# Kernel optimization log

Hardware: AMD Instinct MI355X
Metric: run time of the kernel (lower is better)

The kernel has to match this reference:

```python
import jax, jax.numpy as jnp
import numpy as np

H, L, N = 512, 2048, 64  # channels, seq len, SSM state size


def _make_dplr_hippo(n):
    # make_HiPPO / make_NPLR_HiPPO / make_DPLR_HiPPO from the source
    p0 = np.sqrt(1.0 + 2.0 * np.arange(n))
    A = p0[:, None] * p0[None, :]
    A = np.tril(A) - np.diag(np.arange(n))
    nhippo = -A
    P = np.sqrt(np.arange(n) + 0.5)
    B = np.sqrt(2.0 * np.arange(n) + 1.0)
    S = nhippo + P[:, None] * P[None, :]
    S_diag = np.diagonal(S)
    Lam_re = np.mean(S_diag) * np.ones_like(S_diag)
    Lam_im, V = jnp.linalg.eigh(jnp.asarray(S, jnp.complex64) * (-1j))
    Pc = V.conj().T @ jnp.asarray(P, jnp.complex64)
    Bc = V.conj().T @ jnp.asarray(B, jnp.complex64)
    return (jnp.asarray(Lam_re, jnp.float32), jnp.asarray(Lam_im, jnp.float32),
            Pc, Bc)


def setup_inputs() -> dict:
    key = jax.random.key(0)
    k_u, k_c, k_s = jax.random.split(key, 3)
    Lre, Lim, Pc, Bc = _make_dplr_hippo(N)
    tile = lambda v: jnp.tile(v[None, :], (H, 1)).astype(jnp.float32)  # (H,N)
    return {
        "u": jax.random.normal(k_u, (L, H), dtype=jnp.float32),
        "x0_re": jnp.zeros((N, H), jnp.float32),
        "x0_im": jnp.zeros((N, H), jnp.float32),
        "Lambda_re": tile(Lre),
        "Lambda_im": tile(Lim),
        "P_re": tile(Pc.real), "P_im": tile(Pc.imag),
        "B_re": tile(Bc.real), "B_im": tile(Bc.imag),
        "C": jax.random.normal(k_c, (H, N, 2), jnp.float32) * (0.5 ** 0.5),
        "D": jnp.ones((H, 1), jnp.float32),
        "log_step": jax.random.uniform(k_s, (H, 1), jnp.float32,
                                       minval=np.log(1e-3), maxval=np.log(1e-1)),
    }


def _discretize(Lam, P, B, Ct, step):
    # discrete_DPLR with Q = P (as in setup); per-channel, vmapped over H.
    n = Lam.shape[0]
    I = jnp.eye(n, dtype=jnp.complex64)
    A = jnp.diag(Lam) - P[:, None] * P.conj()[None, :]
    A0 = (2.0 / step) * I + A
    Dd = jnp.diag(1.0 / (2.0 / step - Lam))
    Qc = P.conj()[None, :]            # (1,N)
    P2 = P[:, None]                   # (N,1)
    A1 = Dd - (Dd @ P2) * (1.0 / (1.0 + Qc @ Dd @ P2)) * (Qc @ Dd)
    Ab = A1 @ A0                      # (N,N)
    Bb = 2.0 * (A1 @ B[:, None])[:, 0]
    AbL = jnp.linalg.matrix_power(Ab, L)
    Cb = (Ct[None, :] @ jnp.linalg.inv(I - AbL).conj()).conj()[0]
    return Ab, Bb, Cb


def _forward(u, x0_re, x0_im, Lambda_re, Lambda_im, P_re, P_im,
             B_re, B_im, C, D, log_step):
    Lam = jnp.clip(Lambda_re, None, -0.0001) + 1j * Lambda_im  # (H,N)
    Pc = P_re + 1j * P_im
    Bc = B_re + 1j * B_im
    Cc = C[..., 0] + 1j * C[..., 1]
    step = jnp.exp(log_step)[:, 0]                              # (H,)
    Ab, Bb, Cb = jax.vmap(_discretize)(Lam, Pc, Bc, Cc, step)   # (H,N,N),(H,N),(H,N)

    x0 = jnp.transpose(x0_re + 1j * x0_im)                      # (H,N) complex

    def body(x, u_t):  # x: (H,N) complex, u_t: (H,)
        x = jnp.einsum('hnm,hm->hn', Ab, x) + Bb * u_t[:, None]
        y = jnp.einsum('hn,hn->h', Cb, x)
        return x, y.real

    _, ys = jax.lax.scan(body, x0, u)                           # ys: (L,H)
    return ys + u * D[:, 0][None, :]                            # (L,H) float32


def reference(u, x0_re, x0_im, Lambda_re, Lambda_im, P_re, P_im,
              B_re, B_im, C, D, log_step):
    return _forward(u, x0_re, x0_im, Lambda_re, Lambda_im, P_re, P_im,
                    B_re, B_im, C, D, log_step)
```

## Files before the change

kernel.cpp:

```cpp
#include <hip/hip_runtime.h>

#define HH 512
#define LL 2048
#define NN 64
#define TT 64
#define CC 32
#define NLDA 68
#define SP 72

typedef __attribute__((ext_vector_type(8))) short bf16x8_t;
typedef __attribute__((ext_vector_type(4))) float floatx4;

__device__ __forceinline__ float2 cmul(float2 a, float2 b) {
    return make_float2(a.x * b.x - a.y * b.y, a.x * b.y + a.y * b.x);
}
__device__ __forceinline__ float2 crecip(float2 a) {
    float id = 1.0f / (a.x * a.x + a.y * a.y);
    return make_float2(a.x * id, -a.y * id);
}
template <int CTRL>
__device__ __forceinline__ float dpp_mov(float x) {
    return __int_as_float(__builtin_amdgcn_update_dpp(
        0, __float_as_int(x), CTRL, 0xf, 0xf, true));
}
__device__ __forceinline__ float wave_sum_bcast(float x) {
    x += dpp_mov<0x111>(x);
    x += dpp_mov<0x112>(x);
    x += dpp_mov<0x114>(x);
    x += dpp_mov<0x118>(x);
    x += dpp_mov<0x142>(x);
    x += dpp_mov<0x143>(x);
    return __int_as_float(__builtin_amdgcn_readlane(__float_as_int(x), 63));
}
__device__ __forceinline__ float rlane(float x, int i) {
    return __int_as_float(__builtin_amdgcn_readlane(__float_as_int(x), i));
}
__device__ __forceinline__ unsigned short f2bf(float f) {
    unsigned int u = __float_as_uint(f);
    u += 0x7FFFu + ((u >> 16) & 1u);
    return (unsigned short)(u >> 16);
}
__device__ __forceinline__ float bf2f(unsigned short s) {
    return __uint_as_float(((unsigned int)s) << 16);
}

__device__ __forceinline__ void closed_form(
    int h, int n,
    const float* __restrict__ Lre, const float* __restrict__ Lim,
    const float* __restrict__ Pre, const float* __restrict__ Pim,
    const float* __restrict__ Bre, const float* __restrict__ Bim,
    const float* __restrict__ logstep,
    float2& da, float2& DPv, float2& tv, float2& bb) {
    float step = expf(logstep[h]);
    float as = 2.0f / step;
    float lr = fminf(Lre[h * NN + n], -1e-4f);
    float li = Lim[h * NN + n];
    float2 a = make_float2(as + lr, li);
    float2 Dn = crecip(make_float2(as - lr, -li));
    float2 P = make_float2(Pre[h * NN + n], Pim[h * NN + n]);
    float2 Bv = make_float2(Bre[h * NN + n], Bim[h * NN + n]);
    float2 cP = make_float2(P.x, -P.y);
    float p2 = P.x * P.x + P.y * P.y;
    float2 rt = cmul(cmul(cP, Dn), Bv);
    float2 e = make_float2(wave_sum_bcast(Dn.x * p2), wave_sum_bcast(Dn.y * p2));
    float2 rv = make_float2(wave_sum_bcast(rt.x), wave_sum_bcast(rt.y));
    float2 cc = crecip(make_float2(1.0f + e.x, e.y));
    da = cmul(Dn, a);
    DPv = cmul(Dn, P);
    float2 tmp = cmul(cc, make_float2(da.x - e.x, da.y - e.y));
    tv = cmul(cP, make_float2(1.0f + tmp.x, tmp.y));
    float2 crv = cmul(cc, rv);
    float2 cd = cmul(crv, DPv);
    float2 db = cmul(Dn, Bv);
    bb = make_float2(2.0f * (db.x - cd.x), 2.0f * (db.y - cd.y));
}

__device__ __forceinline__ void pack_tiles(
    unsigned short* mRh, unsigned short* mRl,
    unsigned short* mIh, unsigned short* mIl,
    unsigned short* mTRh, unsigned short* mTRl,
    unsigned short* mTIh, unsigned short* mTIl,
    int w, int lm, int q, const float Cr[4][4], const float Ci[4][4]) {
    #pragma unroll
    for (int nt = 0; nt < 4; ++nt) {
        const int c = nt * 16 + lm;
        unsigned short hr[4], lr_[4], hi_[4], li_[4];
        #pragma unroll
        for (int reg = 0; reg < 4; ++reg) {
            const float xr = Cr[nt][reg], xi = Ci[nt][reg];
            hr[reg] = f2bf(xr); lr_[reg] = f2bf(xr - bf2f(hr[reg]));
            hi_[reg] = f2bf(xi); li_[reg] = f2bf(xi - bf2f(hi_[reg]));
            const int r = 16 * w + 4 * q + reg;
            mRh[r * SP + c] = hr[reg]; mRl[r * SP + c] = lr_[reg];
            mIh[r * SP + c] = hi_[reg]; mIl[r * SP + c] = li_[reg];
        }
        const int tb = c * SP + 16 * w + 4 * q;
        *(ushort4*)&mTRh[tb] = make_ushort4(hr[0], hr[1], hr[2], hr[3]);
        *(ushort4*)&mTRl[tb] = make_ushort4(lr_[0], lr_[1], lr_[2], lr_[3]);
        *(ushort4*)&mTIh[tb] = make_ushort4(hi_[0], hi_[1], hi_[2], hi_[3]);
        *(ushort4*)&mTIl[tb] = make_ushort4(li_[0], li_[1], li_[2], li_[3]);
    }
}

extern "C" __global__ void __launch_bounds__(256, 2)
k_fusedA(const float* __restrict__ Lre, const float* __restrict__ Lim,
         const float* __restrict__ Pre, const float* __restrict__ Pim,
         const float* __restrict__ Bre, const float* __restrict__ Bim,
         const float* __restrict__ Cmat, const float* __restrict__ logstep,
         const float* __restrict__ u,
         float2* __restrict__ wM, float2* __restrict__ wCb,
         float2* __restrict__ wP) {
    extern __shared__ __align__(16) char smem[];
    const int tid = threadIdx.x;

    if (blockIdx.x < HH) {
        const int h = blockIdx.x;
        unsigned short* mRh  = (unsigned short*)smem;
        unsigned short* mRl  = mRh + 64 * SP;
        unsigned short* mIh  = mRl + 64 * SP;
        unsigned short* mIl  = mIh + 64 * SP;
        unsigned short* mTRh = mIl + 64 * SP;
        unsigned short* mTRl = mTRh + 64 * SP;
        unsigned short* mTIh = mTRl + 64 * SP;
        unsigned short* mTIl = mTIh + 64 * SP;
        float* Nr = (float*)smem;
        float* Ni = Nr + 64 * NLDA;
        float2* sda  = (float2*)(smem + 73728);
        float2* sDP  = sda + NN;
        float2* st   = sDP + NN;
        float2* sBb  = st + NN;
        float2* srhs = sBb + NN;
        float2* sx   = srhs + NN;
        float2* pp   = sx + NN;

        const int w = tid >> 6;
        const int lane = tid & 63;
        const int lm = lane & 15, q = lane >> 4;

        if (tid < NN) {
            float2 da, DPv, tv, bb;
            closed_form(h, tid, Lre, Lim, Pre, Pim, Bre, Bim, logstep,
                        da, DPv, tv, bb);
            sda[tid] = da; sDP[tid] = DPv; st[tid] = tv; sBb[tid] = bb;
            srhs[tid] = make_float2(Cmat[h * NN * 2 + tid * 2],
                                    -Cmat[h * NN * 2 + tid * 2 + 1]);
        }
        __syncthreads();

        {
            float Cr[4][4], Ci[4][4];
            #pragma unroll
            for (int nt = 0; nt < 4; ++nt) {
                const int c = nt * 16 + lm;
                const float2 tc = st[c];
                #pragma unroll
                for (int reg = 0; reg < 4; ++reg) {
                    const int r = 16 * w + 4 * q + reg;
                    const float2 dp = sDP[r];
                    float vr = -(dp.x * tc.x - dp.y * tc.y);
                    float vi = -(dp.x * tc.y + dp.y * tc.x);
                    if (r == c) { vr += sda[r].x; vi += sda[r].y; }
                    Cr[nt][reg] = vr; Ci[nt][reg] = vi;
                }
            }
            pack_tiles(mRh, mRl, mIh, mIl, mTRh, mTRl, mTIh, mTIl,
                       w, lm, q, Cr, Ci);
        }
        __syncthreads();

        const int arow = (16 * w + lm) * SP + q * 8;
        for (int it = 0; it < 11; ++it) {
            floatx4 z4 = {0.f, 0.f, 0.f, 0.f};
            floatx4 aP[4] = {z4, z4, z4, z4};
            floatx4 aQ[4] = {z4, z4, z4, z4};
            floatx4 aC[4] = {z4, z4, z4, z4};
            for (int k2 = 0; k2 < 2; ++k2) {
                const int ao = arow + k2 * 32;
                const bf16x8_t ARh = *(const bf16x8_t*)&mRh[ao];
                const bf16x8_t ARl = *(const bf16x8_t*)&mRl[ao];
                const bf16x8_t AIh = *(const bf16x8_t*)&mIh[ao];
                const bf16x8_t AIl = *(const bf16x8_t*)&mIl[ao];
                bf16x8_t BRh[4], BRl[4], BIh[4], BIl[4];
                #pragma unroll
                for (int nt = 0; nt < 4; ++nt) {
                    const int bo = (nt * 16 + lm) * SP + k2 * 32 + q * 8;
                    BRh[nt] = *(const bf16x8_t*)&mTRh[bo];
                    BRl[nt] = *(const bf16x8_t*)&mTRl[bo];
                    BIh[nt] = *(const bf16x8_t*)&mTIh[bo];
                    BIl[nt] = *(const bf16x8_t*)&mTIl[bo];
                }
                #pragma unroll
                for (int nt = 0; nt < 4; ++nt) {
                    aP[nt] = __builtin_amdgcn_mfma_f32_16x16x32_bf16(ARh, BRh[nt], aP[nt], 0, 0, 0);
                    aP[nt] = __builtin_amdgcn_mfma_f32_16x16x32_bf16(ARh, BRl[nt], aP[nt], 0, 0, 0);
                    aP[nt] = __builtin_amdgcn_mfma_f32_16x16x32_bf16(ARl, BRh[nt], aP[nt], 0, 0, 0);
                    aQ[nt] = __builtin_amdgcn_mfma_f32_16x16x32_bf16(AIh, BIh[nt], aQ[nt], 0, 0, 0);
                    aQ[nt] = __builtin_amdgcn_mfma_f32_16x16x32_bf16(AIh, BIl[nt], aQ[nt], 0, 0, 0);
                    aQ[nt] = __builtin_amdgcn_mfma_f32_16x16x32_bf16(AIl, BIh[nt], aQ[nt], 0, 0, 0);
                    aC[nt] = __builtin_amdgcn_mfma_f32_16x16x32_bf16(ARh, BIh[nt], aC[nt], 0, 0, 0);
                    aC[nt] = __builtin_amdgcn_mfma_f32_16x16x32_bf16(ARh, BIl[nt], aC[nt], 0, 0, 0);
                    aC[nt] = __builtin_amdgcn_mfma_f32_16x16x32_bf16(ARl, BIh[nt], aC[nt], 0, 0, 0);
                    aC[nt] = __builtin_amdgcn_mfma_f32_16x16x32_bf16(AIh, BRh[nt], aC[nt], 0, 0, 0);
                    aC[nt] = __builtin_amdgcn_mfma_f32_16x16x32_bf16(AIh, BRl[nt], aC[nt], 0, 0, 0);
                    aC[nt] = __builtin_amdgcn_mfma_f32_16x16x32_bf16(AIl, BRh[nt], aC[nt], 0, 0, 0);
                }
            }
            __syncthreads();
            if (it < 10) {
                float Cr[4][4], Ci[4][4];
                #pragma unroll
                for (int nt = 0; nt < 4; ++nt)
                    #pragma unroll
                    for (int reg = 0; reg < 4; ++reg) {
                        Cr[nt][reg] = aP[nt][reg] - aQ[nt][reg];
                        Ci[nt][reg] = aC[nt][reg];
                    }
                pack_tiles(mRh, mRl, mIh, mIl, mTRh, mTRl, mTIh, mTIl,
                           w, lm, q, Cr, Ci);
                __syncthreads();
                if (it == 5) {
                    for (int idx = tid; idx < NN * NN; idx += 256) {
                        const int c = idx >> 6, k = idx & 63;
                        wM[h * NN * NN + idx] = make_float2(
                            bf2f(mTRh[c * SP + k]) + bf2f(mTRl[c * SP + k]),
                            bf2f(mTIh[c * SP + k]) + bf2f(mTIl[c * SP + k]));
                    }
                }
            } else {
                #pragma unroll
                for (int nt = 0; nt < 4; ++nt) {
                    const int c = nt * 16 + lm;
                    #pragma unroll
                    for (int reg = 0; reg < 4; ++reg) {
                        const int r = 16 * w + 4 * q + reg;
                        Nr[r * NLDA + c] = aP[nt][reg] - aQ[nt][reg];
                        Ni[r * NLDA + c] = aC[nt][reg];
                    }
                }
                __syncthreads();
            }
        }

        if (tid < NN) sx[tid] = srhs[tid];
        __syncthreads();
        for (int itn = 0; itn < 24; ++itn) {
            const int i = tid & 63, qq = tid >> 6;
            float pr = 0.0f, pi = 0.0f;
            #pragma unroll 4
            for (int jj = 0; jj < 16; ++jj) {
                const int j = qq * 16 + jj;
                const float nr = Nr[j * NLDA + i], ni = Ni[j * NLDA + i];
                const float2 xj = sx[j];
                pr += nr * xj.x - ni * xj.y;
                pi += nr * xj.y + ni * xj.x;
            }
            pp[qq * 64 + i] = make_float2(pr, pi);
            __syncthreads();
            if (tid < NN) {
                const float2 a0 = pp[tid], a1 = pp[64 + tid];
                const float2 a2 = pp[128 + tid], a3 = pp[192 + tid];
                sx[tid] = make_float2(
                    srhs[tid].x + a0.x + a1.x + a2.x + a3.x,
                    srhs[tid].y + a0.y + a1.y + a2.y + a3.y);
            }
            __syncthreads();
        }
        if (tid < NN) wCb[h * NN + tid] = sx[tid];
    } else {
        const int h = blockIdx.x - HH;
        float2* sG  = (float2*)smem;
        float*  su  = (float*)(smem + 32768);
        float2* sda = (float2*)(smem + 40960);
        float2* sDP = sda + NN;
        float2* st  = sDP + NN;
        float2* sBb = st + NN;

        const int wv = tid >> 6, lane = tid & 63;
        for (int idx = tid; idx < LL; idx += 256)
            su[idx] = u[idx * HH + h];
        if (tid < NN) {
            float2 da, DPv, tv, bb;
            closed_form(h, tid, Lre, Lim, Pre, Pim, Bre, Bim, logstep,
                        da, DPv, tv, bb);
            sda[tid] = da; sDP[tid] = DPv; st[tid] = tv; sBb[tid] = bb;
        }
        __syncthreads();

        if (tid < 64) {
            const float2 da = sda[lane], DP = sDP[lane], tt = st[lane];
            float Gr = sBb[lane].x, Gi = sBb[lane].y;
            for (int m = 0; m < TT; ++m) {
                sG[m * NN + lane] = make_float2(Gr, Gi);
                float c1 = tt.x * Gr - tt.y * Gi;
                float c2 = tt.x * Gi + tt.y * Gr;
                c1 += dpp_mov<0x111>(c1); c2 += dpp_mov<0x111>(c2);
                c1 += dpp_mov<0x112>(c1); c2 += dpp_mov<0x112>(c2);
                c1 += dpp_mov<0x114>(c1); c2 += dpp_mov<0x114>(c2);
                c1 += dpp_mov<0x118>(c1); c2 += dpp_mov<0x118>(c2);
                c1 += dpp_mov<0x142>(c1); c2 += dpp_mov<0x142>(c2);
                c1 += dpp_mov<0x143>(c1); c2 += dpp_mov<0x143>(c2);
                const float S1 = rlane(c1, 63);
                const float S2 = rlane(c2, 63);
                float nGr = da.x * Gr - da.y * Gi - (DP.x * S1 - DP.y * S2);
                float nGi = da.x * Gi + da.y * Gr - (DP.x * S2 + DP.y * S1);
                Gr = nGr; Gi = nGi;
            }
        }
        __syncthreads();

        float accr[8] = {}, acci[8] = {};
        for (int j = 0; j < TT; ++j) {
            const float2 g = sG[(TT - 1 - j) * NN + lane];
            #pragma unroll
            for (int qc = 0; qc < 8; ++qc) {
                const float uv = su[((wv * 8 + qc) << 6) + j];
                accr[qc] += g.x * uv; acci[qc] += g.y * uv;
            }
        }
        #pragma unroll
        for (int qc = 0; qc < 8; ++qc)
            wP[(h * CC + wv * 8 + qc) * NN + lane] = make_float2(accr[qc], acci[qc]);
    }
}

extern "C" __global__ void __launch_bounds__(256, 2)
k_fusedB(const float* __restrict__ Lre, const float* __restrict__ Lim,
         const float* __restrict__ Pre, const float* __restrict__ Pim,
         const float* __restrict__ Bre, const float* __restrict__ Bim,
         const float* __restrict__ logstep,
         const float* __restrict__ u, const float* __restrict__ Dvec,
         const float* __restrict__ x0_re, const float* __restrict__ x0_im,
         const float2* __restrict__ wM, const float2* __restrict__ wCb,
         const float2* __restrict__ wP, float* __restrict__ out) {
    extern __shared__ __align__(16) char smem[];
    unsigned short* sVr  = (unsigned short*)smem;
    unsigned short* sVi  = (unsigned short*)(smem + 9216);
    unsigned short* sXrh = (unsigned short*)(smem + 18432);
    unsigned short* sXrl = (unsigned short*)(smem + 23040);
    unsigned short* sXih = (unsigned short*)(smem + 27648);
    unsigned short* sXil = (unsigned short*)(smem + 32256);
    float*          su   = (float*)(smem + 36864);
    float*          sK   = (float*)(smem + 45056);
    float*          y0   = (float*)(smem + 45312);

    const int h = blockIdx.x;
    const int tid = threadIdx.x;
    const int wv = tid >> 6, lane = tid & 63;
    const int lm = lane & 15, q = lane >> 4;

    if (wv == 0) {
        float2 da, DP, tt, Bb;
        closed_form(h, lane, Lre, Lim, Pre, Pim, Bre, Bim, logstep,
                    da, DP, tt, Bb);
        const float2 Cb = wCb[h * NN + lane];
        float Gr = Bb.x, Gi = Bb.y;
        float vr = Cb.x, vi = Cb.y;
        for (int m = 0; m < TT; ++m) {
            float ch[5];
            ch[0] = Cb.x * Gr - Cb.y * Gi;
            ch[1] = tt.x * Gr - tt.y * Gi;
            ch[2] = tt.x * Gi + tt.y * Gr;
            ch[3] = vr * DP.x - vi * DP.y;
            ch[4] = vr * DP.y + vi * DP.x;
            #pragma unroll
            for (int c = 0; c < 5; ++c) ch[c] += dpp_mov<0x111>(ch[c]);
            #pragma unroll
            for (int c = 0; c < 5; ++c) ch[c] += dpp_mov<0x112>(ch[c]);
            #pragma unroll
            for (int c = 0; c < 5; ++c) ch[c] += dpp_mov<0x114>(ch[c]);
            #pragma unroll
            for (int c = 0; c < 5; ++c) ch[c] += dpp_mov<0x118>(ch[c]);
            #pragma unroll
            for (int c = 0; c < 5; ++c) ch[c] += dpp_mov<0x142>(ch[c]);
            #pragma unroll
            for (int c = 0; c < 5; ++c) ch[c] += dpp_mov<0x143>(ch[c]);
            const float S0 = rlane(ch[0], 63);
            const float S1 = rlane(ch[1], 63);
            const float S2 = rlane(ch[2], 63);
            const float S3 = rlane(ch[3], 63);
            const float S4 = rlane(ch[4], 63);
            if (lane == 0) sK[m] = S0;
            float nGr = da.x * Gr - da.y * Gi - (DP.x * S1 - DP.y * S2);
            float nGi = da.x * Gi + da.y * Gr - (DP.x * S2 + DP.y * S1);
            Gr = nGr; Gi = nGi;
            float nvr = da.x * vr - da.y * vi - (S3 * tt.x - S4 * tt.y);
            float nvi = da.x * vi + da.y * vr - (S3 * tt.y + S4 * tt.x);
            vr = nvr; vi = nvi;
            sVr[m * SP + lane] = f2bf(vr);
            sVi[m * SP + lane] = f2bf(-vi);
        }
    } else if (wv == 1) {
        float Mr[NN], Mi[NN];
        const float2* __restrict__ wMh = wM + h * NN * NN;
        #pragma unroll
        for (int j = 0; j < NN; ++j) {
            const float2 v = wMh[j * NN + lane];
            Mr[j] = v.x; Mi[j] = v.y;
        }
        float xr = x0_re[lane * HH + h], xi = x0_im[lane * HH + h];
        {
            const unsigned short hr = f2bf(xr), hi_ = f2bf(xi);
            sXrh[lane] = hr;  sXrl[lane] = f2bf(xr - bf2f(hr));
            sXih[lane] = hi_; sXil[lane] = f2bf(xi - bf2f(hi_));
        }
        float2 pe_next = wP[(h * CC + 0) * NN + lane];
        for (int c = 1; c < CC; ++c) {
            const float2 pe = pe_next;
            if (c < CC - 1) pe_next = wP[(h * CC + c) * NN + lane];
            float ar[4] = {0.f, 0.f, 0.f, 0.f};
            float ai[4] = {0.f, 0.f, 0.f, 0.f};
            #pragma unroll
            for (int j = 0; j < NN; ++j) {
                const float xjr = rlane(xr, j);
                const float xji = rlane(xi, j);
                ar[j & 3] = fmaf(Mr[j], xjr, ar[j & 3]);
                ar[j & 3] = fmaf(-Mi[j], xji, ar[j & 3]);
                ai[j & 3] = fmaf(Mr[j], xji, ai[j & 3]);
                ai[j & 3] = fmaf(Mi[j], xjr, ai[j & 3]);
            }
            xr = ((ar[0] + ar[1]) + (ar[2] + ar[3])) + pe.x;
            xi = ((ai[0] + ai[1]) + (ai[2] + ai[3])) + pe.y;
            const unsigned short hr = f2bf(xr), hi_ = f2bf(xi);
            sXrh[c * SP + lane] = hr;  sXrl[c * SP + lane] = f2bf(xr - bf2f(hr));
            sXih[c * SP + lane] = hi_; sXil[c * SP + lane] = f2bf(xi - bf2f(hi_));
        }
    } else {
        for (int idx = tid - 128; idx < LL; idx += 128)
            su[idx] = u[idx * HH + h];
    }
    __syncthreads();

    {
        const float Dh = Dvec[h];
        float acc[8] = {};
        for (int s = 0; s < TT; ++s) {
            const int d = lane - s;
            const float kv = (d >= 0) ? sK[d < 0 ? 0 : d] : 0.0f;
            #pragma unroll
            for (int qc = 0; qc < 8; ++qc)
                acc[qc] += kv * su[((wv * 8 + qc) << 6) + s];
        }
        #pragma unroll
        for (int qc = 0; qc < 8; ++qc) {
            const int c = wv * 8 + qc;
            y0[c * 65 + lane] = acc[qc] + Dh * su[c * 64 + lane];
        }
    }
    __syncthreads();

    floatx4 z4 = {0.f, 0.f, 0.f, 0.f};
    floatx4 acc2[2] = {z4, z4};
    #pragma unroll
    for (int k2 = 0; k2 < 2; ++k2) {
        const int ak = (16 * wv + lm) * SP + k2 * 32 + q * 8;
        const bf16x8_t aVr = *(const bf16x8_t*)&sVr[ak];
        const bf16x8_t aVi = *(const bf16x8_t*)&sVi[ak];
        #pragma unroll
        for (int nt = 0; nt < 2; ++nt) {
            const int bk = (nt * 16 + lm) * SP + k2 * 32 + q * 8;
            const bf16x8_t bRh = *(const bf16x8_t*)&sXrh[bk];
            const bf16x8_t bRl = *(const bf16x8_t*)&sXrl[bk];
            const bf16x8_t bIh = *(const bf16x8_t*)&sXih[bk];
            const bf16x8_t bIl = *(const bf16x8_t*)&sXil[bk];
            acc2[nt] = __builtin_amdgcn_mfma_f32_16x16x32_bf16(aVr, bRh, acc2[nt], 0, 0, 0);
            acc2[nt] = __builtin_amdgcn_mfma_f32_16x16x32_bf16(aVr, bRl, acc2[nt], 0, 0, 0);
            acc2[nt] = __builtin_amdgcn_mfma_f32_16x16x32_bf16(aVi, bIh, acc2[nt], 0, 0, 0);
            acc2[nt] = __builtin_amdgcn_mfma_f32_16x16x32_bf16(aVi, bIl, acc2[nt], 0, 0, 0);
        }
    }
    #pragma unroll
    for (int nt = 0; nt < 2; ++nt) {
        #pragma unroll
        for (int reg = 0; reg < 4; ++reg) {
            const int c = nt * 16 + lm;
            const int t = 16 * wv + 4 * q + reg;
            out[(c * TT + t) * HH + h] = acc2[nt][reg] + y0[c * 65 + t];
        }
    }
}

extern "C" void kernel_launch(void* const* d_in, const int* in_sizes, int n_in,
                              void* d_out, int out_size, void* d_ws, size_t ws_size,
                              hipStream_t stream) {
    const float* u    = (const float*)d_in[0];
    const float* x0re = (const float*)d_in[1];
    const float* x0im = (const float*)d_in[2];
    const float* Lre  = (const float*)d_in[3];
    const float* Lim  = (const float*)d_in[4];
    const float* Pre  = (const float*)d_in[5];
    const float* Pim  = (const float*)d_in[6];
    const float* Bre  = (const float*)d_in[7];
    const float* Bim  = (const float*)d_in[8];
    const float* C    = (const float*)d_in[9];
    const float* Dv   = (const float*)d_in[10];
    const float* lst  = (const float*)d_in[11];

    float2* wM  = (float2*)d_ws;
    float2* wP  = wM + HH * NN * NN;
    float2* wCb = wP + HH * CC * NN;
    float* out = (float*)d_out;

    hipLaunchKernelGGL(k_fusedA, dim3(2 * HH), dim3(256), 78848, stream,
                       Lre, Lim, Pre, Pim, Bre, Bim, C, lst, u,
                       wM, wCb, wP);
    hipLaunchKernelGGL(k_fusedB, dim3(HH), dim3(256), 53632, stream,
                       Lre, Lim, Pre, Pim, Bre, Bim, lst, u, Dv,
                       x0re, x0im, wM, wCb, wP, out);
}
```

Baseline: 227.1 us.

## Move chunk-input state computation into kernel B and cut Neumann iterations

```diff
diff --git a/kernel.cpp b/kernel.cpp
--- a/kernel.cpp
+++ b/kernel.cpp
@@ -107,220 +107,162 @@
          const float* __restrict__ Pre, const float* __restrict__ Pim,
          const float* __restrict__ Bre, const float* __restrict__ Bim,
          const float* __restrict__ Cmat, const float* __restrict__ logstep,
-         const float* __restrict__ u,
-         float2* __restrict__ wM, float2* __restrict__ wCb,
-         float2* __restrict__ wP) {
+         float2* __restrict__ wM, float2* __restrict__ wCb) {
     extern __shared__ __align__(16) char smem[];
     const int tid = threadIdx.x;
-
-    if (blockIdx.x < HH) {
-        const int h = blockIdx.x;
-        unsigned short* mRh  = (unsigned short*)smem;
-        unsigned short* mRl  = mRh + 64 * SP;
-        unsigned short* mIh  = mRl + 64 * SP;
-        unsigned short* mIl  = mIh + 64 * SP;
-        unsigned short* mTRh = mIl + 64 * SP;
-        unsigned short* mTRl = mTRh + 64 * SP;
-        unsigned short* mTIh = mTRl + 64 * SP;
-        unsigned short* mTIl = mTIh + 64 * SP;
-        float* Nr = (float*)smem;
-        float* Ni = Nr + 64 * NLDA;
-        float2* sda  = (float2*)(smem + 73728);
-        float2* sDP  = sda + NN;
-        float2* st   = sDP + NN;
-        float2* sBb  = st + NN;
-        float2* srhs = sBb + NN;
-        float2* sx   = srhs + NN;
-        float2* pp   = sx + NN;
-
-        const int w = tid >> 6;
-        const int lane = tid & 63;
-        const int lm = lane & 15, q = lane >> 4;
-
-        if (tid < NN) {
-            float2 da, DPv, tv, bb;
-            closed_form(h, tid, Lre, Lim, Pre, Pim, Bre, Bim, logstep,
-                        da, DPv, tv, bb);
-            sda[tid] = da; sDP[tid] = DPv; st[tid] = tv; sBb[tid] = bb;
-            srhs[tid] = make_float2(Cmat[h * NN * 2 + tid * 2],
-                                    -Cmat[h * NN * 2 + tid * 2 + 1]);
+    const int h = blockIdx.x;
+
+    unsigned short* mRh  = (unsigned short*)smem;
+    unsigned short* mRl  = mRh + 64 * SP;
+    unsigned short* mIh  = mRl + 64 * SP;
+    unsigned short* mIl  = mIh + 64 * SP;
+    unsigned short* mTRh = mIl + 64 * SP;
+    unsigned short* mTRl = mTRh + 64 * SP;
+    unsigned short* mTIh = mTRl + 64 * SP;
+    unsigned short* mTIl = mTIh + 64 * SP;
+    float* Nr = (float*)smem;
+    float* Ni = Nr + 64 * NLDA;
+    float2* sda  = (float2*)(smem + 73728);
+    float2* sDP  = sda + NN;
+    float2* st   = sDP + NN;
+    float2* sBb  = st + NN;
+    float2* srhs = sBb + NN;
+    float2* sx   = srhs + NN;
+    float2* pp   = sx + NN;
+
+    const int w = tid >> 6;
+    const int lane = tid & 63;
+    const int lm = lane & 15, q = lane >> 4;
+
+    if (tid < NN) {
+        float2 da, DPv, tv, bb;
+        closed_form(h, tid, Lre, Lim, Pre, Pim, Bre, Bim, logstep,
+                    da, DPv, tv, bb);
+        sda[tid] = da; sDP[tid] = DPv; st[tid] = tv; sBb[tid] = bb;
+        srhs[tid] = make_float2(Cmat[h * NN * 2 + tid * 2],
+                                -Cmat[h * NN * 2 + tid * 2 + 1]);
+    }
+    __syncthreads();
+
+    {
+        float Cr[4][4], Ci[4][4];
+        #pragma unroll
+        for (int nt = 0; nt < 4; ++nt) {
+            const int c = nt * 16 + lm;
+            const float2 tc = st[c];
+            #pragma unroll
+            for (int reg = 0; reg < 4; ++reg) {
+                const int r = 16 * w + 4 * q + reg;
+                const float2 dp = sDP[r];
+                float vr = -(dp.x * tc.x - dp.y * tc.y);
+                float vi = -(dp.x * tc.y + dp.y * tc.x);
+                if (r == c) { vr += sda[r].x; vi += sda[r].y; }
+                Cr[nt][reg] = vr; Ci[nt][reg] = vi;
+            }
+        }
+        pack_tiles(mRh, mRl, mIh, mIl, mTRh, mTRl, mTIh, mTIl,
+                   w, lm, q, Cr, Ci);
+    }
+    __syncthreads();
+
+    const int arow = (16 * w + lm) * SP + q * 8;
+    for (int it = 0; it < 11; ++it) {
+        floatx4 z4 = {0.f, 0.f, 0.f, 0.f};
+        floatx4 aP[4] = {z4, z4, z4, z4};
+        floatx4 aQ[4] = {z4, z4, z4, z4};
+        floatx4 aC[4] = {z4, z4, z4, z4};
+        for (int k2 = 0; k2 < 2; ++k2) {
+            const int ao = arow + k2 * 32;
+            const bf16x8_t ARh = *(const bf16x8_t*)&mRh[ao];
+            const bf16x8_t ARl = *(const bf16x8_t*)&mRl[ao];
+            const bf16x8_t AIh = *(const bf16x8_t*)&mIh[ao];
+            const bf16x8_t AIl = *(const bf16x8_t*)&mIl[ao];
+            bf16x8_t BRh[4], BRl[4], BIh[4], BIl[4];
+            #pragma unroll
+            for (int nt = 0; nt < 4; ++nt) {
+                const int bo = (nt * 16 + lm) * SP + k2 * 32 + q * 8;
+                BRh[nt] = *(const bf16x8_t*)&mTRh[bo];
+                BRl[nt] = *(const bf16x8_t*)&mTRl[bo];
+                BIh[nt] = *(const bf16x8_t*)&mTIh[bo];
+                BIl[nt] = *(const bf16x8_t*)&mTIl[bo];
+            }
+            #pragma unroll
+            for (int nt = 0; nt < 4; ++nt) {
+                aP[nt] = __builtin_amdgcn_mfma_f32_16x16x32_bf16(ARh, BRh[nt], aP[nt], 0, 0, 0);
+                aP[nt] = __builtin_amdgcn_mfma_f32_16x16x32_bf16(ARh, BRl[nt], aP[nt], 0, 0, 0);
+                aP[nt] = __builtin_amdgcn_mfma_f32_16x16x32_bf16(ARl, BRh[nt], aP[nt], 0, 0, 0);
+                aQ[nt] = __builtin_amdgcn_mfma_f32_16x16x32_bf16(AIh, BIh[nt], aQ[nt], 0, 0, 0);
+                aQ[nt] = __builtin_amdgcn_mfma_f32_16x16x32_bf16(AIh, BIl[nt], aQ[nt], 0, 0, 0);
+                aQ[nt] = __builtin_amdgcn_mfma_f32_16x16x32_bf16(AIl, BIh[nt], aQ[nt], 0, 0, 0);
+                aC[nt] = __builtin_amdgcn_mfma_f32_16x16x32_bf16(ARh, BIh[nt], aC[nt], 0, 0, 0);
+                aC[nt] = __builtin_amdgcn_mfma_f32_16x16x32_bf16(ARh, BIl[nt], aC[nt], 0, 0, 0);
+                aC[nt] = __builtin_amdgcn_mfma_f32_16x16x32_bf16(ARl, BIh[nt], aC[nt], 0, 0, 0);
+                aC[nt] = __builtin_amdgcn_mfma_f32_16x16x32_bf16(AIh, BRh[nt], aC[nt], 0, 0, 0);
+                aC[nt] = __builtin_amdgcn_mfma_f32_16x16x32_bf16(AIh, BRl[nt], aC[nt], 0, 0, 0);
+                aC[nt] = __builtin_amdgcn_mfma_f32_16x16x32_bf16(AIl, BRh[nt], aC[nt], 0, 0, 0);
+            }
         }
         __syncthreads();
-
-        {
+        if (it < 10) {
             float Cr[4][4], Ci[4][4];
+            #pragma unroll
+            for (int nt = 0; nt < 4; ++nt)
+                #pragma unroll
+                for (int reg = 0; reg < 4; ++reg) {
+                    Cr[nt][reg] = aP[nt][reg] - aQ[nt][reg];
+                    Ci[nt][reg] = aC[nt][reg];
+                }
+            pack_tiles(mRh, mRl, mIh, mIl, mTRh, mTRl, mTIh, mTIl,
+                       w, lm, q, Cr, Ci);
+            __syncthreads();
+            if (it == 5) {
+                for (int idx = tid; idx < NN * NN; idx += 256) {
+                    const int c = idx >> 6, k = idx & 63;
+                    wM[h * NN * NN + idx] = make_float2(
+                        bf2f(mTRh[c * SP + k]) + bf2f(mTRl[c * SP + k]),
+                        bf2f(mTIh[c * SP + k]) + bf2f(mTIl[c * SP + k]));
+                }
+            }
+        } else {
             #pragma unroll
             for (int nt = 0; nt < 4; ++nt) {
                 const int c = nt * 16 + lm;
-                const float2 tc = st[c];
                 #pragma unroll
                 for (int reg = 0; reg < 4; ++reg) {
                     const int r = 16 * w + 4 * q + reg;
-                    const float2 dp = sDP[r];
-                    float vr = -(dp.x * tc.x - dp.y * tc.y);
-                    float vi = -(dp.x * tc.y + dp.y * tc.x);
-                    if (r == c) { vr += sda[r].x; vi += sda[r].y; }
-                    Cr[nt][reg] = vr; Ci[nt][reg] = vi;
+                    Nr[r * NLDA + c] = aP[nt][reg] - aQ[nt][reg];
+                    Ni[r * NLDA + c] = aC[nt][reg];
                 }
             }
-            pack_tiles(mRh, mRl, mIh, mIl, mTRh, mTRl, mTIh, mTIl,
-                       w, lm, q, Cr, Ci);
-        }
+            __syncthreads();
+        }
+    }
+
+    if (tid < NN) sx[tid] = srhs[tid];
+    __syncthreads();
+    for (int itn = 0; itn < 16; ++itn) {
+        const int i = tid & 63, qq = tid >> 6;
+        float pr = 0.0f, pi = 0.0f;
+        #pragma unroll 4
+        for (int jj = 0; jj < 16; ++jj) {
+            const int j = qq * 16 + jj;
+            const float nr = Nr[j * NLDA + i], ni = Ni[j * NLDA + i];
+            const float2 xj = sx[j];
+            pr += nr * xj.x - ni * xj.y;
+            pi += nr * xj.y + ni * xj.x;
+        }
+        pp[qq * 64 + i] = make_float2(pr, pi);
         __syncthreads();
-
-        const int arow = (16 * w + lm) * SP + q * 8;
-        for (int it = 0; it < 11; ++it) {
-            floatx4 z4 = {0.f, 0.f, 0.f, 0.f};
-            floatx4 aP[4] = {z4, z4, z4, z4};
-            floatx4 aQ[4] = {z4, z4, z4, z4};
-            floatx4 aC[4] = {z4, z4, z4, z4};
-            for (int k2 = 0; k2 < 2; ++k2) {
-                const int ao = arow + k2 * 32;
-                const bf16x8_t ARh = *(const bf16x8_t*)&mRh[ao];
-                const bf16x8_t ARl = *(const bf16x8_t*)&mRl[ao];
-                const bf16x8_t AIh = *(const bf16x8_t*)&mIh[ao];
-                const bf16x8_t AIl = *(const bf16x8_t*)&mIl[ao];
-                bf16x8_t BRh[4], BRl[4], BIh[4], BIl[4];
-                #pragma unroll
-                for (int nt = 0; nt < 4; ++nt) {
-                    const int bo = (nt * 16 + lm) * SP + k2 * 32 + q * 8;
-                    BRh[nt] = *(const bf16x8_t*)&mTRh[bo];
-                    BRl[nt] = *(const bf16x8_t*)&mTRl[bo];
-                    BIh[nt] = *(const bf16x8_t*)&mTIh[bo];
-                    BIl[nt] = *(const bf16x8_t*)&mTIl[bo];
-                }
-                #pragma unroll
-                for (int nt = 0; nt < 4; ++nt) {
-                    aP[nt] = __builtin_amdgcn_mfma_f32_16x16x32_bf16(ARh, BRh[nt], aP[nt], 0, 0, 0);
-                    aP[nt] = __builtin_amdgcn_mfma_f32_16x16x32_bf16(ARh, BRl[nt], aP[nt], 0, 0, 0);
-                    aP[nt] = __builtin_amdgcn_mfma_f32_16x16x32_bf16(ARl, BRh[nt], aP[nt], 0, 0, 0);
-                    aQ[nt] = __builtin_amdgcn_mfma_f32_16x16x32_bf16(AIh, BIh[nt], aQ[nt], 0, 0, 0);
-                    aQ[nt] = __builtin_amdgcn_mfma_f32_16x16x32_bf16(AIh, BIl[nt], aQ[nt], 0, 0, 0);
-                    aQ[nt] = __builtin_amdgcn_mfma_f32_16x16x32_bf16(AIl, BIh[nt], aQ[nt], 0, 0, 0);
-                    aC[nt] = __builtin_amdgcn_mfma_f32_16x16x32_bf16(ARh, BIh[nt], aC[nt], 0, 0, 0);
-                    aC[nt] = __builtin_amdgcn_mfma_f32_16x16x32_bf16(ARh, BIl[nt], aC[nt], 0, 0, 0);
-                    aC[nt] = __builtin_amdgcn_mfma_f32_16x16x32_bf16(ARl, BIh[nt], aC[nt], 0, 0, 0);
-                    aC[nt] = __builtin_amdgcn_mfma_f32_16x16x32_bf16(AIh, BRh[nt], aC[nt], 0, 0, 0);
-                    aC[nt] = __builtin_amdgcn_mfma_f32_16x16x32_bf16(AIh, BRl[nt], aC[nt], 0, 0, 0);
-                    aC[nt] = __builtin_amdgcn_mfma_f32_16x16x32_bf16(AIl, BRh[nt], aC[nt], 0, 0, 0);
-                }
-            }
-            __syncthreads();
-            if (it < 10) {
-                float Cr[4][4], Ci[4][4];
-                #pragma unroll
-                for (int nt = 0; nt < 4; ++nt)
-                    #pragma unroll
-                    for (int reg = 0; reg < 4; ++reg) {
-                        Cr[nt][reg] = aP[nt][reg] - aQ[nt][reg];
-                        Ci[nt][reg] = aC[nt][reg];
-                    }
-                pack_tiles(mRh, mRl, mIh, mIl, mTRh, mTRl, mTIh, mTIl,
-                           w, lm, q, Cr, Ci);
-                __syncthreads();
-                if (it == 5) {
-                    for (int idx = tid; idx < NN * NN; idx += 256) {
-                        const int c = idx >> 6, k = idx & 63;
-                        wM[h * NN * NN + idx] = make_float2(
-                            bf2f(mTRh[c * SP + k]) + bf2f(mTRl[c * SP + k]),
-                            bf2f(mTIh[c * SP + k]) + bf2f(mTIl[c * SP + k]));
-                    }
-                }
-            } else {
-                #pragma unroll
-                for (int nt = 0; nt < 4; ++nt) {
-                    const int c = nt * 16 + lm;
-                    #pragma unroll
-                    for (int reg = 0; reg < 4; ++reg) {
-                        const int r = 16 * w + 4 * q + reg;
-                        Nr[r * NLDA + c] = aP[nt][reg] - aQ[nt][reg];
-                        Ni[r * NLDA + c] = aC[nt][reg];
-                    }
-                }
-                __syncthreads();
-            }
-        }
-
-        if (tid < NN) sx[tid] = srhs[tid];
+        if (tid < NN) {
+            const float2 a0 = pp[tid], a1 = pp[64 + tid];
+            const float2 a2 = pp[128 + tid], a3 = pp[192 + tid];
+            sx[tid] = make_float2(
+                srhs[tid].x + a0.x + a1.x + a2.x + a3.x,
+                srhs[tid].y + a0.y + a1.y + a2.y + a3.y);
+        }
         __syncthreads();
-        for (int itn = 0; itn < 24; ++itn) {
-            const int i = tid & 63, qq = tid >> 6;
-            float pr = 0.0f, pi = 0.0f;
-            #pragma unroll 4
-            for (int jj = 0; jj < 16; ++jj) {
-                const int j = qq * 16 + jj;
-                const float nr = Nr[j * NLDA + i], ni = Ni[j * NLDA + i];
-                const float2 xj = sx[j];
-                pr += nr * xj.x - ni * xj.y;
-                pi += nr * xj.y + ni * xj.x;
-            }
-            pp[qq * 64 + i] = make_float2(pr, pi);
-            __syncthreads();
-            if (tid < NN) {
-                const float2 a0 = pp[tid], a1 = pp[64 + tid];
-                const float2 a2 = pp[128 + tid], a3 = pp[192 + tid];
-                sx[tid] = make_float2(
-                    srhs[tid].x + a0.x + a1.x + a2.x + a3.x,
-                    srhs[tid].y + a0.y + a1.y + a2.y + a3.y);
-            }
-            __syncthreads();
-        }
-        if (tid < NN) wCb[h * NN + tid] = sx[tid];
-    } else {
-        const int h = blockIdx.x - HH;
-        float2* sG  = (float2*)smem;
-        float*  su  = (float*)(smem + 32768);
-        float2* sda = (float2*)(smem + 40960);
-        float2* sDP = sda + NN;
-        float2* st  = sDP + NN;
-        float2* sBb = st + NN;
-
-        const int wv = tid >> 6, lane = tid & 63;
-        for (int idx = tid; idx < LL; idx += 256)
-            su[idx] = u[idx * HH + h];
-        if (tid < NN) {
-            float2 da, DPv, tv, bb;
-            closed_form(h, tid, Lre, Lim, Pre, Pim, Bre, Bim, logstep,
-                        da, DPv, tv, bb);
-            sda[tid] = da; sDP[tid] = DPv; st[tid] = tv; sBb[tid] = bb;
-        }
-        __syncthreads();
-
-        if (tid < 64) {
-            const float2 da = sda[lane], DP = sDP[lane], tt = st[lane];
-            float Gr = sBb[lane].x, Gi = sBb[lane].y;
-            for (int m = 0; m < TT; ++m) {
-                sG[m * NN + lane] = make_float2(Gr, Gi);
-                float c1 = tt.x * Gr - tt.y * Gi;
-                float c2 = tt.x * Gi + tt.y * Gr;
-                c1 += dpp_mov<0x111>(c1); c2 += dpp_mov<0x111>(c2);
-                c1 += dpp_mov<0x112>(c1); c2 += dpp_mov<0x112>(c2);
-                c1 += dpp_mov<0x114>(c1); c2 += dpp_mov<0x114>(c2);
-                c1 += dpp_mov<0x118>(c1); c2 += dpp_mov<0x118>(c2);
-                c1 += dpp_mov<0x142>(c1); c2 += dpp_mov<0x142>(c2);
-                c1 += dpp_mov<0x143>(c1); c2 += dpp_mov<0x143>(c2);
-                const float S1 = rlane(c1, 63);
-                const float S2 = rlane(c2, 63);
-                float nGr = da.x * Gr - da.y * Gi - (DP.x * S1 - DP.y * S2);
-                float nGi = da.x * Gi + da.y * Gr - (DP.x * S2 + DP.y * S1);
-                Gr = nGr; Gi = nGi;
-            }
-        }
-        __syncthreads();
-
-        float accr[8] = {}, acci[8] = {};
-        for (int j = 0; j < TT; ++j) {
-            const float2 g = sG[(TT - 1 - j) * NN + lane];
-            #pragma unroll
-            for (int qc = 0; qc < 8; ++qc) {
-                const float uv = su[((wv * 8 + qc) << 6) + j];
-                accr[qc] += g.x * uv; acci[qc] += g.y * uv;
-            }
-        }
-        #pragma unroll
-        for (int qc = 0; qc < 8; ++qc)
-            wP[(h * CC + wv * 8 + qc) * NN + lane] = make_float2(accr[qc], acci[qc]);
-    }
+    }
+    if (tid < NN) wCb[h * NN + tid] = sx[tid];
 }
 
 extern "C" __global__ void __launch_bounds__(256, 2)
@@ -331,7 +273,7 @@
          const float* __restrict__ u, const float* __restrict__ Dvec,
          const float* __restrict__ x0_re, const float* __restrict__ x0_im,
          const float2* __restrict__ wM, const float2* __restrict__ wCb,
-         const float2* __restrict__ wP, float* __restrict__ out) {
+         float* __restrict__ out) {
     extern __shared__ __align__(16) char smem[];
     unsigned short* sVr  = (unsigned short*)smem;
     unsigned short* sVi  = (unsigned short*)(smem + 9216);
@@ -342,11 +284,15 @@
     float*          su   = (float*)(smem + 36864);
     float*          sK   = (float*)(smem + 45056);
     float*          y0   = (float*)(smem + 45312);
+    float2*         sP   = (float2*)(smem + 53632);
 
     const int h = blockIdx.x;
     const int tid = threadIdx.x;
     const int wv = tid >> 6, lane = tid & 63;
     const int lm = lane & 15, q = lane >> 4;
+
+    float Mr[NN], Mi[NN];
+    float x0r = 0.0f, x0i = 0.0f;
 
     if (wv == 0) {
         float2 da, DP, tt, Bb;
@@ -390,23 +336,66 @@
             sVi[m * SP + lane] = f2bf(-vi);
         }
     } else if (wv == 1) {
-        float Mr[NN], Mi[NN];
         const float2* __restrict__ wMh = wM + h * NN * NN;
         #pragma unroll
         for (int j = 0; j < NN; ++j) {
             const float2 v = wMh[j * NN + lane];
             Mr[j] = v.x; Mi[j] = v.y;
         }
-        float xr = x0_re[lane * HH + h], xi = x0_im[lane * HH + h];
+        x0r = x0_re[lane * HH + h];
+        x0i = x0_im[lane * HH + h];
+    } else {
+        const int par = wv - 2;
+        for (int k = lane; k < 1024; k += 64) {
+            const int cc = ((k >> 6) << 1) | par;
+            const int s = k & 63;
+            su[cc * 64 + s] = u[(cc * 64 + s) * HH + h];
+        }
+        float2 da, DP, tt, Bb;
+        closed_form(h, lane, Lre, Lim, Pre, Pim, Bre, Bim, logstep,
+                    da, DP, tt, Bb);
+        float Gr = Bb.x, Gi = Bb.y;
+        float ar[16] = {}, ai[16] = {};
+        for (int m = 0; m < TT; ++m) {
+            #pragma unroll
+            for (int ci = 0; ci < 16; ++ci) {
+                const int cc = (ci << 1) | par;
+                const float uv = su[cc * 64 + (63 - m)];
+                ar[ci] = fmaf(Gr, uv, ar[ci]);
+                ai[ci] = fmaf(Gi, uv, ai[ci]);
+            }
+            float c1 = tt.x * Gr - tt.y * Gi;
+            float c2 = tt.x * Gi + tt.y * Gr;
+            c1 += dpp_mov<0x111>(c1); c2 += dpp_mov<0x111>(c2);
+            c1 += dpp_mov<0x112>(c1); c2 += dpp_mov<0x112>(c2);
+            c1 += dpp_mov<0x114>(c1); c2 += dpp_mov<0x114>(c2);
+            c1 += dpp_mov<0x118>(c1); c2 += dpp_mov<0x118>(c2);
+            c1 += dpp_mov<0x142>(c1); c2 += dpp_mov<0x142>(c2);
+            c1 += dpp_mov<0x143>(c1); c2 += dpp_mov<0x143>(c2);
+            const float S1 = rlane(c1, 63);
+            const float S2 = rlane(c2, 63);
+            float nGr = da.x * Gr - da.y * Gi - (DP.x * S1 - DP.y * S2);
+            float nGi = da.x * Gi + da.y * Gr - (DP.x * S2 + DP.y * S1);
+            Gr = nGr; Gi = nGi;
+        }
+        #pragma unroll
+        for (int ci = 0; ci < 16; ++ci) {
+            const int cc = (ci << 1) | par;
+            sP[cc * 64 + lane] = make_float2(ar[ci], ai[ci]);
+        }
+    }
+    __syncthreads();
+
+    const float Dh = Dvec[h];
+    if (wv == 1) {
+        float xr = x0r, xi = x0i;
         {
             const unsigned short hr = f2bf(xr), hi_ = f2bf(xi);
             sXrh[lane] = hr;  sXrl[lane] = f2bf(xr - bf2f(hr));
             sXih[lane] = hi_; sXil[lane] = f2bf(xi - bf2f(hi_));
         }
-        float2 pe_next = wP[(h * CC + 0) * NN + lane];
         for (int c = 1; c < CC; ++c) {
-            const float2 pe = pe_next;
-            if (c < CC - 1) pe_next = wP[(h * CC + c) * NN + lane];
+            const float2 pe = sP[(c - 1) * 64 + lane];
             float ar[4] = {0.f, 0.f, 0.f, 0.f};
             float ai[4] = {0.f, 0.f, 0.f, 0.f};
             #pragma unroll
@@ -425,25 +414,16 @@
             sXih[c * SP + lane] = hi_; sXil[c * SP + lane] = f2bf(xi - bf2f(hi_));
         }
     } else {
-        for (int idx = tid - 128; idx < LL; idx += 128)
-            su[idx] = u[idx * HH + h];
-    }
-    __syncthreads();
-
-    {
-        const float Dh = Dvec[h];
-        float acc[8] = {};
-        for (int s = 0; s < TT; ++s) {
-            const int d = lane - s;
-            const float kv = (d >= 0) ? sK[d < 0 ? 0 : d] : 0.0f;
-            #pragma unroll
-            for (int qc = 0; qc < 8; ++qc)
-                acc[qc] += kv * su[((wv * 8 + qc) << 6) + s];
-        }
-        #pragma unroll
-        for (int qc = 0; qc < 8; ++qc) {
-            const int c = wv * 8 + qc;
-            y0[c * 65 + lane] = acc[qc] + Dh * su[c * 64 + lane];
+        const int c0 = (wv == 0) ? 0 : (wv == 2 ? 11 : 22);
+        const int c1 = (wv == 0) ? 11 : (wv == 2 ? 22 : 32);
+        for (int c = c0; c < c1; ++c) {
+            float acc = 0.0f;
+            for (int s = 0; s < TT; ++s) {
+                const int d = lane - s;
+                const float kv = (d >= 0) ? sK[d < 0 ? 0 : d] : 0.0f;
+                acc = fmaf(kv, su[c * 64 + s], acc);
+            }
+            y0[c * 65 + lane] = acc + Dh * su[c * 64 + lane];
         }
     }
     __syncthreads();
@@ -496,14 +476,13 @@
     const float* lst  = (const float*)d_in[11];
 
     float2* wM  = (float2*)d_ws;
-    float2* wP  = wM + HH * NN * NN;
-    float2* wCb = wP + HH * CC * NN;
+    float2* wCb = wM + HH * NN * NN;
     float* out = (float*)d_out;
 
-    hipLaunchKernelGGL(k_fusedA, dim3(2 * HH), dim3(256), 78848, stream,
-                       Lre, Lim, Pre, Pim, Bre, Bim, C, lst, u,
-                       wM, wCb, wP);
-    hipLaunchKernelGGL(k_fusedB, dim3(HH), dim3(256), 53632, stream,
+    hipLaunchKernelGGL(k_fusedA, dim3(HH), dim3(256), 78848, stream,
+                       Lre, Lim, Pre, Pim, Bre, Bim, C, lst,
+                       wM, wCb);
+    hipLaunchKernelGGL(k_fusedB, dim3(HH), dim3(256), 70016, stream,
                        Lre, Lim, Pre, Pim, Bre, Bim, lst, u, Dv,
-                       x0re, x0im, wM, wCb, wP, out);
-}
+                       x0re, x0im, wM, wCb, out);
+}
```

After: 205.4 us. 1.11x faster.
